# Optimization experiments

Hardware: AMD Instinct MI355X
Metric: run time of the kernel (lower is better)

The kernel has to match this reference:

```python
import jax, jax.numpy as jnp
import numpy as np

B, T, D, H, E = 4, 2048, 1024, 1024, 8
NEG_SLOPE = 0.01  # torch LeakyReLU default

def leaky_relu(x):
    return jnp.where(x >= 0, x, NEG_SLOPE * x)

def setup_inputs() -> dict:
    key = jax.random.key(0)
    ks = jax.random.split(key, 10)
    s = 0.02
    return {
        "x": jax.random.normal(ks[0], (B, T, D), jnp.float32),
        "gate_w": jax.random.normal(ks[1], (D, E), jnp.float32) * s,
        "gate_b": jnp.zeros((E,), jnp.float32),
        "w1": jax.random.normal(ks[2], (E, D, H), jnp.float32) * s,
        "b1": jnp.zeros((E, H), jnp.float32),
        "w2": jax.random.normal(ks[3], (E, H, H), jnp.float32) * s,
        "b2": jnp.zeros((E, H), jnp.float32),
        "w3": jax.random.normal(ks[4], (E, H, D), jnp.float32) * s,
        "b3": jnp.zeros((E, D), jnp.float32),
        "topn": 2,
    }

def reference(x, gate_w, gate_b, w1, b1, w2, b2, w3, b3, topn):
    # Gating: softmax over experts, top-k mask, L1 renormalize
    gating = jax.nn.softmax(x @ gate_w + gate_b, axis=-1)          # [B,T,E]
    _, topk_idx = jax.lax.top_k(gating, topn)                       # [B,T,k]
    mask = jax.nn.one_hot(topk_idx, E, dtype=gating.dtype).sum(-2)  # [B,T,E]
    g = gating * mask
    g = g / jnp.maximum(jnp.sum(jnp.abs(g), axis=-1, keepdims=True), 1e-12)
    # Dense all-expert MLP: Linear -> LeakyReLU -> Linear -> LeakyReLU -> Linear
    h = leaky_relu(jnp.einsum('btd,edh->bteh', x, w1) + b1)         # [B,T,E,H]
    h = leaky_relu(jnp.einsum('bteh,ehg->bteg', h, w2) + b2)        # [B,T,E,H]
    eo = jnp.einsum('bteh,ehd->bted', h, w3) + b3                   # [B,T,E,D]
    # Weighted combine
    return jnp.einsum('bte,bted->btd', g, eo)                       # [B,T,D]
```

## Files before the change

kernel.cpp:

```cpp
#include <hip/hip_runtime.h>
#include <hip/hip_bf16.h>
#include <stdint.h>

#define TOKENS   8192
#define DDIM     1024
#define EXPERTS  8
#define NSLOT    (TOKENS * 2)

typedef __bf16 bf16x8_t __attribute__((ext_vector_type(8)));
typedef __bf16 bf16x4_t __attribute__((ext_vector_type(4)));
typedef float  f32x4_t  __attribute__((ext_vector_type(4)));

__device__ __forceinline__ void gl_lds16(const void* g, void* l) {
  __builtin_amdgcn_global_load_lds(
      (const __attribute__((address_space(1))) void*)g,
      (__attribute__((address_space(3))) void*)l, 16, 0, 0);
}

__global__ void twt_k(const float* __restrict__ w, __bf16* __restrict__ wT) {
  __shared__ float tile[64][33];
  const int kb = blockIdx.x * 64, nb = blockIdx.y * 32;
  const size_t ebase = (size_t)blockIdx.z << 20;
  const int tx = threadIdx.x, ty = threadIdx.y;
  const float* src = w + ebase;
#pragma unroll
  for (int r = ty; r < 64; r += 8)
    tile[r][tx] = src[(size_t)(kb + r) * 1024 + nb + tx];
  __syncthreads();
  __bf16* dst = wT + ebase;
#pragma unroll
  for (int r = ty; r < 32; r += 8) {
    union { __bf16 h[2]; unsigned u; } pk;
    pk.h[0] = (__bf16)tile[2 * tx][r];
    pk.h[1] = (__bf16)tile[2 * tx + 1][r];
    *(unsigned*)(dst + (size_t)(nb + r) * 1024 + kb + 2 * tx) = pk.u;
  }
}

__global__ __launch_bounds__(256) void gate_k(
    const float* __restrict__ x, const float* __restrict__ gw,
    const float* __restrict__ gb, __bf16* __restrict__ xbf,
    int* __restrict__ top_i, float* __restrict__ top_w) {
  const int t = blockIdx.x * 4 + (threadIdx.x >> 6);
  const int lane = threadIdx.x & 63;
  const float* xr = x + (size_t)t * DDIM;
  __bf16* xo = xbf + (size_t)t * DDIM;
  float acc[EXPERTS];
#pragma unroll
  for (int e = 0; e < EXPERTS; ++e) acc[e] = 0.f;
  for (int d = lane; d < DDIM; d += 64) {
    const float xv = xr[d];
    xo[d] = (__bf16)xv;
    const float4 g0 = ((const float4*)gw)[d * 2];
    const float4 g1 = ((const float4*)gw)[d * 2 + 1];
    acc[0] += xv * g0.x; acc[1] += xv * g0.y;
    acc[2] += xv * g0.z; acc[3] += xv * g0.w;
    acc[4] += xv * g1.x; acc[5] += xv * g1.y;
    acc[6] += xv * g1.z; acc[7] += xv * g1.w;
  }
#pragma unroll
  for (int e = 0; e < EXPERTS; ++e)
    for (int s = 32; s > 0; s >>= 1) acc[e] += __shfl_down(acc[e], s);
  if (lane == 0) {
#pragma unroll
    for (int e = 0; e < EXPERTS; ++e) acc[e] += gb[e];
    int i1 = 0;
    for (int e = 1; e < EXPERTS; ++e)
      if (acc[e] > acc[i1]) i1 = e;
    int i2 = (i1 == 0) ? 1 : 0;
    for (int e = 0; e < EXPERTS; ++e)
      if (e != i1 && acc[e] > acc[i2]) i2 = e;
    const float r = expf(acc[i2] - acc[i1]);
    const float wA = 1.f / (1.f + r);
    const float wB = r / (1.f + r);
    top_i[t * 2] = i1; top_i[t * 2 + 1] = i2;
    top_w[t * 2] = wA; top_w[t * 2 + 1] = wB;
  }
}

__global__ __launch_bounds__(1024) void plan_k(const int* __restrict__ top_i,
                                               int* __restrict__ eoff,
                                               int* __restrict__ tok_list,
                                               int* __restrict__ slot_of) {
  const int tid = threadIdx.x;
  const int lane = tid & 63, wid = tid >> 6;
  __shared__ int ws[16][EXPERTS];
  __shared__ int eoff_s[EXPERTS];
  __shared__ int base_lds[1024 * EXPERTS];

  int ids[16];
  unsigned long long h64 = 0;
#pragma unroll
  for (int j = 0; j < 16; ++j) {
    ids[j] = top_i[tid * 16 + j];
    h64 += 1ull << (ids[j] * 8);
  }
#pragma unroll
  for (int e = 0; e < EXPERTS; ++e) {
    const int h = (int)((h64 >> (8 * e)) & 0xff);
    int v = h;
    for (int s = 1; s < 64; s <<= 1) {
      const int u = __shfl_up(v, s);
      if (lane >= s) v += u;
    }
    const int excl = v - h;
    const int tot = __shfl(v, 63);
    if (lane == 0) ws[wid][e] = tot;
    base_lds[tid * EXPERTS + e] = excl;
  }
  __syncthreads();
  if (tid == 0) {
    int tot[EXPERTS];
    for (int e = 0; e < EXPERTS; ++e) {
      int run = 0;
      for (int w = 0; w < 16; ++w) { const int c = ws[w][e]; ws[w][e] = run; run += c; }
      tot[e] = run;
    }
    int s = 0;
    for (int e = 0; e < EXPERTS; ++e) { eoff_s[e] = s; eoff[e] = s; s += tot[e]; }
    eoff[EXPERTS] = s;
  }
  __syncthreads();
#pragma unroll
  for (int e = 0; e < EXPERTS; ++e)
    base_lds[tid * EXPERTS + e] += eoff_s[e] + ws[wid][e];
  unsigned long long pre64 = 0;
#pragma unroll
  for (int j = 0; j < 16; ++j) {
    const int entry = tid * 16 + j;
    const int e = ids[j];
    const int pre = (int)((pre64 >> (8 * e)) & 0xff);
    pre64 += 1ull << (8 * e);
    const int s = base_lds[tid * EXPERTS + e] + pre;
    tok_list[s] = entry >> 1;
    slot_of[entry] = s;
  }
}

template <int GATHER, int LEAKY, int OUTBF>
__global__ __launch_bounds__(256) void moe_gemm(
    const __bf16* __restrict__ A, const int* __restrict__ tok,
    const __bf16* __restrict__ W, const float* __restrict__ bias,
    const int* __restrict__ eoff, __bf16* __restrict__ outb,
    float* __restrict__ outf) {
  const int e = blockIdx.z;
  const int off = eoff[e];
  const int ne = eoff[e + 1] - off;
  const int m0 = blockIdx.y * 128;
  if (m0 >= ne) return;
  const int n0 = blockIdx.x * 128;

  __shared__ __align__(16) __bf16 As[128 * 32];
  __shared__ __align__(16) __bf16 Bs[128 * 32];

  const int tid = threadIdx.x;
  const int lane = tid & 63;
  const int wid = tid >> 6;
  const int wm = wid >> 1, wn = wid & 1;
  const int ln = lane & 15, quad = lane >> 4;

  const __bf16* aptr[2];
  const __bf16* bptr[2];
  __bf16* alds[2];
  __bf16* blds[2];
#pragma unroll
  for (int j = 0; j < 2; ++j) {
    const int c = (wid * 2 + j) * 64 + lane;
    const int row = c >> 2, kc = c & 3;
    int r = m0 + row;
    if (r >= ne) r = m0;
    const long arow = GATHER ? (long)tok[off + r] : (long)(off + r);
    aptr[j] = A + arow * DDIM + kc * 8;
    alds[j] = (__bf16*)As + (wid * 2 + j) * 512;
    bptr[j] = W + ((long)e << 20) + (long)(n0 + row) * 1024 + kc * 8;
    blds[j] = (__bf16*)Bs + (wid * 2 + j) * 512;
  }

  const f32x4_t vzero = {0.f, 0.f, 0.f, 0.f};
  f32x4_t acc[4][4];
#pragma unroll
  for (int i = 0; i < 4; ++i)
#pragma unroll
    for (int j = 0; j < 4; ++j) acc[i][j] = vzero;

  for (int kt = 0; kt < 32; ++kt) {
    const int k0 = kt * 32;
    __syncthreads();
    gl_lds16(aptr[0] + k0, alds[0]);
    gl_lds16(aptr[1] + k0, alds[1]);
    gl_lds16(bptr[0] + k0, blds[0]);
    gl_lds16(bptr[1] + k0, blds[1]);
    __syncthreads();

    bf16x8_t aF[4], bF[4];
#pragma unroll
    for (int i = 0; i < 4; ++i)
      aF[i] = *(const bf16x8_t*)(As + (wm * 64 + i * 16 + ln) * 32 + quad * 8);
#pragma unroll
    for (int j = 0; j < 4; ++j)
      bF[j] = *(const bf16x8_t*)(Bs + (wn * 64 + j * 16 + ln) * 32 + quad * 8);
#pragma unroll
    for (int i = 0; i < 4; ++i)
#pragma unroll
      for (int j = 0; j < 4; ++j)
        acc[i][j] = __builtin_amdgcn_mfma_f32_16x16x32_bf16(aF[i], bF[j],
                                                            acc[i][j], 0, 0, 0);
  }

  const float* bs = bias + e * 1024;
#pragma unroll
  for (int i = 0; i < 4; ++i) {
    const int rloc = wm * 64 + i * 16 + quad * 4;
#pragma unroll
    for (int j = 0; j < 4; ++j) {
      const int col = n0 + wn * 64 + j * 16 + ln;
      const float bv = bs[col];
#pragma unroll
      for (int r = 0; r < 4; ++r) {
        const int m = m0 + rloc + r;
        if (m < ne) {
          float v = acc[i][j][r] + bv;
          if (LEAKY) v = (v >= 0.f) ? v : 0.01f * v;
          if (OUTBF)
            outb[(size_t)(off + m) * 1024 + col] = (__bf16)v;
          else
            outf[(size_t)(off + m) * 1024 + col] = v;
        }
      }
    }
  }
}

__global__ __launch_bounds__(256) void combine_k(
    const float* __restrict__ eo, const int* __restrict__ slot_of,
    const float* __restrict__ top_w, float* __restrict__ out) {
  const int t = blockIdx.x;
  const int s1 = slot_of[t * 2], s2 = slot_of[t * 2 + 1];
  const float w1 = top_w[t * 2], w2 = top_w[t * 2 + 1];
  const float4 a = ((const float4*)(eo + (size_t)s1 * DDIM))[threadIdx.x];
  const float4 b = ((const float4*)(eo + (size_t)s2 * DDIM))[threadIdx.x];
  float4 o;
  o.x = w1 * a.x + w2 * b.x;
  o.y = w1 * a.y + w2 * b.y;
  o.z = w1 * a.z + w2 * b.z;
  o.w = w1 * a.w + w2 * b.w;
  ((float4*)(out + (size_t)t * DDIM))[threadIdx.x] = o;
}

extern "C" void kernel_launch(void* const* d_in, const int* in_sizes, int n_in,
                              void* d_out, int out_size, void* d_ws,
                              size_t ws_size, hipStream_t stream) {
  (void)in_sizes; (void)n_in; (void)out_size; (void)ws_size;
  const float* x  = (const float*)d_in[0];
  const float* gw = (const float*)d_in[1];
  const float* gb = (const float*)d_in[2];
  const float* w1 = (const float*)d_in[3];
  const float* b1 = (const float*)d_in[4];
  const float* w2 = (const float*)d_in[5];
  const float* b2 = (const float*)d_in[6];
  const float* w3 = (const float*)d_in[7];
  const float* b3 = (const float*)d_in[8];
  float* out = (float*)d_out;

  uint8_t* p = (uint8_t*)d_ws;
  auto alloc = [&](size_t b) {
    uint8_t* r = p;
    p += (b + 255) & ~(size_t)255;
    return r;
  };
  int*    eoff     = (int*)alloc(4 * (EXPERTS + 1));
  int*    top_i    = (int*)alloc(4ull * TOKENS * 2);
  float*  top_w    = (float*)alloc(4ull * TOKENS * 2);
  int*    slot_of  = (int*)alloc(4ull * TOKENS * 2);
  int*    tok_list = (int*)alloc(4ull * NSLOT);
  __bf16* xbf      = (__bf16*)alloc(2ull * TOKENS * DDIM);
  __bf16* w1T      = (__bf16*)alloc(2ull * EXPERTS * 1024 * 1024);
  __bf16* w2T      = (__bf16*)alloc(2ull * EXPERTS * 1024 * 1024);
  __bf16* w3T      = (__bf16*)alloc(2ull * EXPERTS * 1024 * 1024);
  __bf16* h1       = (__bf16*)alloc(2ull * NSLOT * 1024);
  __bf16* h2       = (__bf16*)alloc(2ull * NSLOT * 1024);
  float*  eo       = (float*)alloc(4ull * NSLOT * 1024);

  gate_k<<<TOKENS / 4, 256, 0, stream>>>(x, gw, gb, xbf, top_i, top_w);
  twt_k<<<dim3(16, 32, EXPERTS), dim3(32, 8), 0, stream>>>(w1, w1T);
  twt_k<<<dim3(16, 32, EXPERTS), dim3(32, 8), 0, stream>>>(w2, w2T);
  twt_k<<<dim3(16, 32, EXPERTS), dim3(32, 8), 0, stream>>>(w3, w3T);
  plan_k<<<1, 1024, 0, stream>>>(top_i, eoff, tok_list, slot_of);

  moe_gemm<1, 1, 1><<<dim3(8, 64, EXPERTS), 256, 0, stream>>>(
      xbf, tok_list, w1T, b1, eoff, h1, nullptr);
  moe_gemm<0, 1, 1><<<dim3(8, 64, EXPERTS), 256, 0, stream>>>(
      h1, nullptr, w2T, b2, eoff, h2, nullptr);
  moe_gemm<0, 0, 0><<<dim3(8, 64, EXPERTS), 256, 0, stream>>>(
      h2, nullptr, w3T, b3, eoff, nullptr, eo);

  combine_k<<<TOKENS, 256, 0, stream>>>(eo, slot_of, top_w, out);
}
```

Baseline: 440.6 us.

## Fuse combine into last GEMM, compact tile worklist, swizzle LDS, merge transposes

The last expert GEMM now scales its output by the gate weight and atomically adds it into the zeroed output, which drops the fp32 expert-output buffer and the separate combine kernel. The planning kernel builds a compact list of (expert, m-tile) work items, so the GEMM grid holds only real tiles instead of many early-exit blocks. LDS loads and reads use an XOR swizzle on the k-chunk to cut bank conflicts. The three weight transposes become one launch and the gate kernel uses float4 loads. The costs are float atomic contention, a memset of the output, and summation order that is no longer fixed.

Result: slower. 504.4 us (+14.5%).

```diff
diff --git a/kernel.cpp b/kernel.cpp
--- a/kernel.cpp
+++ b/kernel.cpp
@@ -6,6 +6,7 @@
 #define DDIM     1024
 #define EXPERTS  8
 #define NSLOT    (TOKENS * 2)
+#define MAXTILE  136
 
 typedef __bf16 bf16x8_t __attribute__((ext_vector_type(8)));
 typedef __bf16 bf16x4_t __attribute__((ext_vector_type(4)));
@@ -17,10 +18,15 @@
       (__attribute__((address_space(3))) void*)l, 16, 0, 0);
 }
 
-__global__ void twt_k(const float* __restrict__ w, __bf16* __restrict__ wT) {
+__global__ void twt_k(const float* __restrict__ w1, const float* __restrict__ w2,
+                      const float* __restrict__ w3, __bf16* __restrict__ w1T,
+                      __bf16* __restrict__ w2T, __bf16* __restrict__ w3T) {
   __shared__ float tile[64][33];
+  const int layer = blockIdx.z >> 3, e = blockIdx.z & 7;
+  const float* w = (layer == 0) ? w1 : (layer == 1) ? w2 : w3;
+  __bf16* wT = (layer == 0) ? w1T : (layer == 1) ? w2T : w3T;
   const int kb = blockIdx.x * 64, nb = blockIdx.y * 32;
-  const size_t ebase = (size_t)blockIdx.z << 20;
+  const size_t ebase = (size_t)e << 20;
   const int tx = threadIdx.x, ty = threadIdx.y;
   const float* src = w + ebase;
 #pragma unroll
@@ -43,20 +49,31 @@
     int* __restrict__ top_i, float* __restrict__ top_w) {
   const int t = blockIdx.x * 4 + (threadIdx.x >> 6);
   const int lane = threadIdx.x & 63;
-  const float* xr = x + (size_t)t * DDIM;
-  __bf16* xo = xbf + (size_t)t * DDIM;
+  const float4* x4 = (const float4*)(x + (size_t)t * DDIM);
+  bf16x4_t* xo4 = (bf16x4_t*)(xbf + (size_t)t * DDIM);
+  const float4* g4 = (const float4*)gw;
   float acc[EXPERTS];
 #pragma unroll
   for (int e = 0; e < EXPERTS; ++e) acc[e] = 0.f;
-  for (int d = lane; d < DDIM; d += 64) {
-    const float xv = xr[d];
-    xo[d] = (__bf16)xv;
-    const float4 g0 = ((const float4*)gw)[d * 2];
-    const float4 g1 = ((const float4*)gw)[d * 2 + 1];
-    acc[0] += xv * g0.x; acc[1] += xv * g0.y;
-    acc[2] += xv * g0.z; acc[3] += xv * g0.w;
-    acc[4] += xv * g1.x; acc[5] += xv * g1.y;
-    acc[6] += xv * g1.z; acc[7] += xv * g1.w;
+#pragma unroll
+  for (int d4 = lane; d4 < 256; d4 += 64) {
+    const float4 v = x4[d4];
+    bf16x4_t o = {(__bf16)v.x, (__bf16)v.y, (__bf16)v.z, (__bf16)v.w};
+    xo4[d4] = o;
+    const float4* g = g4 + (size_t)d4 * 8;
+    float4 ga, gbv;
+    ga = g[0]; gbv = g[1];
+    acc[0] += v.x * ga.x; acc[1] += v.x * ga.y; acc[2] += v.x * ga.z; acc[3] += v.x * ga.w;
+    acc[4] += v.x * gbv.x; acc[5] += v.x * gbv.y; acc[6] += v.x * gbv.z; acc[7] += v.x * gbv.w;
+    ga = g[2]; gbv = g[3];
+    acc[0] += v.y * ga.x; acc[1] += v.y * ga.y; acc[2] += v.y * ga.z; acc[3] += v.y * ga.w;
+    acc[4] += v.y * gbv.x; acc[5] += v.y * gbv.y; acc[6] += v.y * gbv.z; acc[7] += v.y * gbv.w;
+    ga = g[4]; gbv = g[5];
+    acc[0] += v.z * ga.x; acc[1] += v.z * ga.y; acc[2] += v.z * ga.z; acc[3] += v.z * ga.w;
+    acc[4] += v.z * gbv.x; acc[5] += v.z * gbv.y; acc[6] += v.z * gbv.z; acc[7] += v.z * gbv.w;
+    ga = g[6]; gbv = g[7];
+    acc[0] += v.w * ga.x; acc[1] += v.w * ga.y; acc[2] += v.w * ga.z; acc[3] += v.w * ga.w;
+    acc[4] += v.w * gbv.x; acc[5] += v.w * gbv.y; acc[6] += v.w * gbv.z; acc[7] += v.w * gbv.w;
   }
 #pragma unroll
   for (int e = 0; e < EXPERTS; ++e)
@@ -78,10 +95,11 @@
   }
 }
 
-__global__ __launch_bounds__(1024) void plan_k(const int* __restrict__ top_i,
-                                               int* __restrict__ eoff,
-                                               int* __restrict__ tok_list,
-                                               int* __restrict__ slot_of) {
+__global__ __launch_bounds__(1024) void plan_k(
+    const int* __restrict__ top_i, const float* __restrict__ top_w,
+    int* __restrict__ eoff, int* __restrict__ tok_list,
+    int* __restrict__ slot_of, float* __restrict__ slot_w,
+    int* __restrict__ work, int* __restrict__ ntiles) {
   const int tid = threadIdx.x;
   const int lane = tid & 63, wid = tid >> 6;
   __shared__ int ws[16][EXPERTS];
@@ -116,9 +134,14 @@
       for (int w = 0; w < 16; ++w) { const int c = ws[w][e]; ws[w][e] = run; run += c; }
       tot[e] = run;
     }
-    int s = 0;
-    for (int e = 0; e < EXPERTS; ++e) { eoff_s[e] = s; eoff[e] = s; s += tot[e]; }
+    int s = 0, nt = 0;
+    for (int e = 0; e < EXPERTS; ++e) {
+      eoff_s[e] = s; eoff[e] = s; s += tot[e];
+      const int mt = (tot[e] + 127) >> 7;
+      for (int i = 0; i < mt; ++i) work[nt++] = (e << 16) | i;
+    }
     eoff[EXPERTS] = s;
+    ntiles[0] = nt;
   }
   __syncthreads();
 #pragma unroll
@@ -134,20 +157,23 @@
     const int s = base_lds[tid * EXPERTS + e] + pre;
     tok_list[s] = entry >> 1;
     slot_of[entry] = s;
-  }
-}
-
-template <int GATHER, int LEAKY, int OUTBF>
+    slot_w[s] = top_w[entry];
+  }
+}
+
+template <int GATHER, int LEAKY, int COMBINE>
 __global__ __launch_bounds__(256) void moe_gemm(
     const __bf16* __restrict__ A, const int* __restrict__ tok,
     const __bf16* __restrict__ W, const float* __restrict__ bias,
-    const int* __restrict__ eoff, __bf16* __restrict__ outb,
-    float* __restrict__ outf) {
-  const int e = blockIdx.z;
+    const int* __restrict__ eoff, const int* __restrict__ work,
+    const int* __restrict__ ntiles, const float* __restrict__ slot_w,
+    __bf16* __restrict__ outb, float* __restrict__ outf) {
+  if ((int)blockIdx.y >= ntiles[0]) return;
+  const int wk = work[blockIdx.y];
+  const int e = wk >> 16;
+  const int m0 = (wk & 0xffff) * 128;
   const int off = eoff[e];
   const int ne = eoff[e + 1] - off;
-  const int m0 = blockIdx.y * 128;
-  if (m0 >= ne) return;
   const int n0 = blockIdx.x * 128;
 
   __shared__ __align__(16) __bf16 As[128 * 32];
@@ -166,7 +192,8 @@
 #pragma unroll
   for (int j = 0; j < 2; ++j) {
     const int c = (wid * 2 + j) * 64 + lane;
-    const int row = c >> 2, kc = c & 3;
+    const int row = c >> 2;
+    const int kc = (c & 3) ^ ((row >> 1) & 3);
     int r = m0 + row;
     if (r >= ne) r = m0;
     const long arow = GATHER ? (long)tok[off + r] : (long)(off + r);
@@ -175,6 +202,8 @@
     bptr[j] = W + ((long)e << 20) + (long)(n0 + row) * 1024 + kc * 8;
     blds[j] = (__bf16*)Bs + (wid * 2 + j) * 512;
   }
+
+  const int swz = (quad ^ ((ln >> 1) & 3)) * 8;
 
   const f32x4_t vzero = {0.f, 0.f, 0.f, 0.f};
   f32x4_t acc[4][4];
@@ -195,10 +224,10 @@
     bf16x8_t aF[4], bF[4];
 #pragma unroll
     for (int i = 0; i < 4; ++i)
-      aF[i] = *(const bf16x8_t*)(As + (wm * 64 + i * 16 + ln) * 32 + quad * 8);
+      aF[i] = *(const bf16x8_t*)(As + (wm * 64 + i * 16 + ln) * 32 + swz);
 #pragma unroll
     for (int j = 0; j < 4; ++j)
-      bF[j] = *(const bf16x8_t*)(Bs + (wn * 64 + j * 16 + ln) * 32 + quad * 8);
+      bF[j] = *(const bf16x8_t*)(Bs + (wn * 64 + j * 16 + ln) * 32 + swz);
 #pragma unroll
     for (int i = 0; i < 4; ++i)
 #pragma unroll
@@ -221,30 +250,17 @@
         if (m < ne) {
           float v = acc[i][j][r] + bv;
           if (LEAKY) v = (v >= 0.f) ? v : 0.01f * v;
-          if (OUTBF)
+          if (COMBINE) {
+            const int t = tok[off + m];
+            const float w = slot_w[off + m];
+            atomicAdd(&outf[(size_t)t * 1024 + col], w * v);
+          } else {
             outb[(size_t)(off + m) * 1024 + col] = (__bf16)v;
-          else
-            outf[(size_t)(off + m) * 1024 + col] = v;
+          }
         }
       }
     }
   }
-}
-
-__global__ __launch_bounds__(256) void combine_k(
-    const float* __restrict__ eo, const int* __restrict__ slot_of,
-    const float* __restrict__ top_w, float* __restrict__ out) {
-  const int t = blockIdx.x;
-  const int s1 = slot_of[t * 2], s2 = slot_of[t * 2 + 1];
-  const float w1 = top_w[t * 2], w2 = top_w[t * 2 + 1];
-  const float4 a = ((const float4*)(eo + (size_t)s1 * DDIM))[threadIdx.x];
-  const float4 b = ((const float4*)(eo + (size_t)s2 * DDIM))[threadIdx.x];
-  float4 o;
-  o.x = w1 * a.x + w2 * b.x;
-  o.y = w1 * a.y + w2 * b.y;
-  o.z = w1 * a.z + w2 * b.z;
-  o.w = w1 * a.w + w2 * b.w;
-  ((float4*)(out + (size_t)t * DDIM))[threadIdx.x] = o;
 }
 
 extern "C" void kernel_launch(void* const* d_in, const int* in_sizes, int n_in,
@@ -269,9 +285,12 @@
     return r;
   };
   int*    eoff     = (int*)alloc(4 * (EXPERTS + 1));
+  int*    ntiles   = (int*)alloc(4);
+  int*    work     = (int*)alloc(4 * MAXTILE);
   int*    top_i    = (int*)alloc(4ull * TOKENS * 2);
   float*  top_w    = (float*)alloc(4ull * TOKENS * 2);
   int*    slot_of  = (int*)alloc(4ull * TOKENS * 2);
+  float*  slot_w   = (float*)alloc(4ull * NSLOT);
   int*    tok_list = (int*)alloc(4ull * NSLOT);
   __bf16* xbf      = (__bf16*)alloc(2ull * TOKENS * DDIM);
   __bf16* w1T      = (__bf16*)alloc(2ull * EXPERTS * 1024 * 1024);
@@ -279,20 +298,18 @@
   __bf16* w3T      = (__bf16*)alloc(2ull * EXPERTS * 1024 * 1024);
   __bf16* h1       = (__bf16*)alloc(2ull * NSLOT * 1024);
   __bf16* h2       = (__bf16*)alloc(2ull * NSLOT * 1024);
-  float*  eo       = (float*)alloc(4ull * NSLOT * 1024);
+
+  hipMemsetAsync(out, 0, 4ull * TOKENS * DDIM, stream);
 
   gate_k<<<TOKENS / 4, 256, 0, stream>>>(x, gw, gb, xbf, top_i, top_w);
-  twt_k<<<dim3(16, 32, EXPERTS), dim3(32, 8), 0, stream>>>(w1, w1T);
-  twt_k<<<dim3(16, 32, EXPERTS), dim3(32, 8), 0, stream>>>(w2, w2T);
-  twt_k<<<dim3(16, 32, EXPERTS), dim3(32, 8), 0, stream>>>(w3, w3T);
-  plan_k<<<1, 1024, 0, stream>>>(top_i, eoff, tok_list, slot_of);
-
-  moe_gemm<1, 1, 1><<<dim3(8, 64, EXPERTS), 256, 0, stream>>>(
-      xbf, tok_list, w1T, b1, eoff, h1, nullptr);
-  moe_gemm<0, 1, 1><<<dim3(8, 64, EXPERTS), 256, 0, stream>>>(
-      h1, nullptr, w2T, b2, eoff, h2, nullptr);
-  moe_gemm<0, 0, 0><<<dim3(8, 64, EXPERTS), 256, 0, stream>>>(
-      h2, nullptr, w3T, b3, eoff, nullptr, eo);
-
-  combine_k<<<TOKENS, 256, 0, stream>>>(eo, slot_of, top_w, out);
-}
+  twt_k<<<dim3(16, 32, 24), dim3(32, 8), 0, stream>>>(w1, w2, w3, w1T, w2T, w3T);
+  plan_k<<<1, 1024, 0, stream>>>(top_i, top_w, eoff, tok_list, slot_of, slot_w,
+                                 work, ntiles);
+
+  moe_gemm<1, 1, 0><<<dim3(8, MAXTILE), 256, 0, stream>>>(
+      xbf, tok_list, w1T, b1, eoff, work, ntiles, slot_w, h1, nullptr);
+  moe_gemm<0, 1, 0><<<dim3(8, MAXTILE), 256, 0, stream>>>(
+      h1, tok_list, w2T, b2, eoff, work, ntiles, slot_w, h2, nullptr);
+  moe_gemm<0, 0, 1><<<dim3(8, MAXTILE), 256, 0, stream>>>(
+      h2, tok_list, w3T, b3, eoff, work, ntiles, slot_w, nullptr, out);
+}
```
